# Optimization experiments

Hardware: AMD Instinct MI355X
Metric: run time of the kernel (lower is better)

## Reference

```python
import jax, jax.numpy as jnp
import numpy as np

NUM_ANGLES = 360
IMAGE_SIZE = 256
BATCH = 8


def _radon_forward(x, num_angles=NUM_ANGLES):
    # x: [B, 1, D, D]; replicates torch affine_grid + grid_sample(bilinear,
    # padding_mode='zeros', align_corners=False) followed by mean over rows.
    B = x.shape[0]
    D = x.shape[-1]
    img = x[:, 0]  # [B, D, D]
    angles = jnp.linspace(0.0, 180.0, num_angles + 1, dtype=x.dtype)[:-1]
    t = jnp.deg2rad(angles)
    c, s = jnp.cos(t), jnp.sin(t)
    # align_corners=False normalized pixel-center coords in [-1, 1]
    coords = (2.0 * jnp.arange(D, dtype=x.dtype) + 1.0) / D - 1.0
    xw = coords[None, None, :]   # output x (width)
    yh = coords[None, :, None]   # output y (height)
    cN = c[:, None, None]
    sN = s[:, None, None]
    # theta = [[c, -s, 0], [s, c, 0]] applied to (x_out, y_out, 1)
    gx = cN * xw - sN * yh       # [A, D, D]
    gy = sN * xw + cN * yh
    # unnormalize (align_corners=False)
    ix = ((gx + 1.0) * D - 1.0) * 0.5
    iy = ((gy + 1.0) * D - 1.0) * 0.5
    x0 = jnp.floor(ix)
    y0 = jnp.floor(iy)
    x1 = x0 + 1.0
    y1 = y0 + 1.0
    wx1 = ix - x0
    wx0 = 1.0 - wx1
    wy1 = iy - y0
    wy0 = 1.0 - wy1
    img_flat = img.reshape(B, D * D)

    def corner(xc, yc, w):
        valid = (xc >= 0) & (xc <= D - 1) & (yc >= 0) & (yc <= D - 1)
        xi = jnp.clip(xc, 0, D - 1).astype(jnp.int32)
        yi = jnp.clip(yc, 0, D - 1).astype(jnp.int32)
        lin = yi * D + xi                      # [A, D, D]
        vals = img_flat[:, lin]                # [B, A, D, D]
        return vals * (w * valid.astype(x.dtype))[None]

    rotated = (corner(x0, y0, wx0 * wy0) + corner(x1, y0, wx1 * wy0)
               + corner(x0, y1, wx0 * wy1) + corner(x1, y1, wx1 * wy1))
    proj = rotated.mean(axis=2)                # mean over rows (H) -> [B, A, D]
    return proj[:, None]                       # [B, 1, A, D]


def setup_inputs() -> dict:
    key = jax.random.key(0)
    x = jax.random.normal(key, (BATCH, 1, IMAGE_SIZE, IMAGE_SIZE), dtype=jnp.float32)
    return {"x": x}


def reference(x) -> jnp.ndarray:
    return _radon_forward(x)
```

## Files before the change

### kernel.cpp

```cpp
#include <hip/hip_runtime.h>

#define DD 256
#define BB 8
#define NA 360
#define CH 8
#define HC (DD / CH)
#define TS 32

__device__ __forceinline__ unsigned bf16_rne(float f) {
    unsigned u = __float_as_uint(f);
    return (u + 0x7fffu + ((u >> 16) & 1u)) >> 16;
}
__device__ __forceinline__ unsigned pack2(float a, float b) {
    return bf16_rne(a) | (bf16_rne(b) << 16);
}
__device__ __forceinline__ void ufma(uint4 q, float wgt, float* acc) {
    acc[0] = fmaf(__uint_as_float(q.x << 16),          wgt, acc[0]);
    acc[1] = fmaf(__uint_as_float(q.x & 0xffff0000u),  wgt, acc[1]);
    acc[2] = fmaf(__uint_as_float(q.y << 16),          wgt, acc[2]);
    acc[3] = fmaf(__uint_as_float(q.y & 0xffff0000u),  wgt, acc[3]);
    acc[4] = fmaf(__uint_as_float(q.z << 16),          wgt, acc[4]);
    acc[5] = fmaf(__uint_as_float(q.z & 0xffff0000u),  wgt, acc[5]);
    acc[6] = fmaf(__uint_as_float(q.w << 16),          wgt, acc[6]);
    acc[7] = fmaf(__uint_as_float(q.w & 0xffff0000u),  wgt, acc[7]);
}

__global__ __launch_bounds__(256) void pack_bf16(const float* __restrict__ x,
                                                 uint4* __restrict__ pN,
                                                 uint4* __restrict__ pT) {
    __shared__ uint4 t[TS][TS + 1];
    const int tx = threadIdx.x & 31;
    const int ty = threadIdx.x >> 5;
    const int x0 = (blockIdx.x & 7) * TS;
    const int y0 = (blockIdx.x >> 3) * TS;

#pragma unroll
    for (int r = ty; r < TS; r += 8) {
        const int pix = (y0 + r) * DD + x0 + tx;
        uint4 v;
        v.x = pack2(x[0 * DD * DD + pix], x[1 * DD * DD + pix]);
        v.y = pack2(x[2 * DD * DD + pix], x[3 * DD * DD + pix]);
        v.z = pack2(x[4 * DD * DD + pix], x[5 * DD * DD + pix]);
        v.w = pack2(x[6 * DD * DD + pix], x[7 * DD * DD + pix]);
        pN[pix] = v;
        t[r][tx] = v;
    }
    __syncthreads();
#pragma unroll
    for (int r = ty; r < TS; r += 8)
        pT[(x0 + r) * DD + y0 + tx] = t[tx][r];
}

__global__ __launch_bounds__(256) void radon_bf16(const uint4* __restrict__ pN,
                                                  const uint4* __restrict__ pT,
                                                  float* __restrict__ out) {
    const int a  = blockIdx.x;
    const int hc = blockIdx.y;
    const int w  = threadIdx.x;

    const float ang = (float)a * 0.5f;
    const float t = ang * 0.017453292519943295f;
    const float s = sinf(t);
    const float c = cosf(t);

    const float uw  = (float)w - 127.5f;
    const float axN = fmaf(c, uw, 127.5f);
    const float ayN = fmaf(s, uw, 127.5f);

    const uint4* __restrict__ P;
    float ax, dx, ay, dy;
    if (fabsf(s) <= fabsf(c)) { P = pN; ax = axN; dx = -s; ay = ayN; dy = c;  }
    else                      { P = pT; ax = ayN; dx = c;  ay = axN; dy = -s; }

    float acc[BB];
#pragma unroll
    for (int b = 0; b < BB; ++b) acc[b] = 0.f;

    const int h0 = hc * HC;
#pragma unroll 2
    for (int i = 0; i < HC; ++i) {
        const float uh = (float)(h0 + i) - 127.5f;
        const float ix = fmaf(dx, uh, ax);
        const float iy = fmaf(dy, uh, ay);
        const float x0f = floorf(ix), y0f = floorf(iy);
        const float wx1 = ix - x0f, wy1 = iy - y0f;
        const float wx0 = 1.f - wx1, wy0 = 1.f - wy1;
        const int x0 = (int)x0f, y0 = (int)y0f;
        const float vx0 = ((unsigned)x0 < 256u) ? wx0 : 0.f;
        const float vx1 = ((unsigned)(x0 + 1) < 256u) ? wx1 : 0.f;
        const float vy0 = ((unsigned)y0 < 256u) ? wy0 : 0.f;
        const float vy1 = ((unsigned)(y0 + 1) < 256u) ? wy1 : 0.f;
        const int x0c = min(max(x0, 0), 255);
        const int x1c = min(max(x0 + 1, 0), 255);
        const int y0c = min(max(y0, 0), 255);
        const int y1c = min(max(y0 + 1, 0), 255);
        const float w00 = vx0 * vy0, w10 = vx1 * vy0;
        const float w01 = vx0 * vy1, w11 = vx1 * vy1;

        const uint4 q00 = P[y0c * DD + x0c];
        const uint4 q10 = P[y0c * DD + x1c];
        const uint4 q01 = P[y1c * DD + x0c];
        const uint4 q11 = P[y1c * DD + x1c];

        ufma(q00, w00, acc);
        ufma(q10, w10, acc);
        ufma(q01, w01, acc);
        ufma(q11, w11, acc);
    }

    const float sc = 1.0f / 256.0f;
#pragma unroll
    for (int b = 0; b < BB; ++b)
        atomicAdd(out + (size_t)b * NA * DD + (size_t)a * DD + w, acc[b] * sc);
}

__global__ __launch_bounds__(256) void radon_direct(const float* __restrict__ x,
                                                    float* __restrict__ out) {
    const int a  = blockIdx.x;
    const int hc = blockIdx.y;
    const int w  = threadIdx.x;
    const float ang = (float)a * 0.5f;
    const float t = ang * 0.017453292519943295f;
    const float s = sinf(t);
    const float c = cosf(t);
    const float uw = (float)w - 127.5f;
    const float ax = fmaf(c, uw, 127.5f);
    const float ay = fmaf(s, uw, 127.5f);

    float acc[BB];
#pragma unroll
    for (int b = 0; b < BB; ++b) acc[b] = 0.f;

    const int h0 = hc * HC;
    for (int i = 0; i < HC; ++i) {
        const float uh = (float)(h0 + i) - 127.5f;
        const float ix = fmaf(-s, uh, ax);
        const float iy = fmaf(c, uh, ay);
        const float x0f = floorf(ix), y0f = floorf(iy);
        const float wx1 = ix - x0f, wy1 = iy - y0f;
        const float wx0 = 1.f - wx1, wy0 = 1.f - wy1;
        const int x0 = (int)x0f, y0 = (int)y0f;
        const float vx0 = ((unsigned)x0 < 256u) ? wx0 : 0.f;
        const float vx1 = ((unsigned)(x0 + 1) < 256u) ? wx1 : 0.f;
        const float vy0 = ((unsigned)y0 < 256u) ? wy0 : 0.f;
        const float vy1 = ((unsigned)(y0 + 1) < 256u) ? wy1 : 0.f;
        const int x0c = min(max(x0, 0), 255);
        const int x1c = min(max(x0 + 1, 0), 255);
        const int y0c = min(max(y0, 0), 255);
        const int y1c = min(max(y0 + 1, 0), 255);
        const float w00 = vx0 * vy0, w10 = vx1 * vy0;
        const float w01 = vx0 * vy1, w11 = vx1 * vy1;
        const int l00 = y0c * DD + x0c, l10 = y0c * DD + x1c;
        const int l01 = y1c * DD + x0c, l11 = y1c * DD + x1c;
#pragma unroll
        for (int b = 0; b < BB; ++b) {
            const float* ib = x + (size_t)b * DD * DD;
            acc[b] = fmaf(ib[l00], w00, acc[b]);
            acc[b] = fmaf(ib[l10], w10, acc[b]);
            acc[b] = fmaf(ib[l01], w01, acc[b]);
            acc[b] = fmaf(ib[l11], w11, acc[b]);
        }
    }

    const float sc = 1.0f / 256.0f;
    float* o = out + (size_t)a * DD + w;
#pragma unroll
    for (int b = 0; b < BB; ++b)
        atomicAdd(o + (size_t)b * NA * DD, acc[b] * sc);
}

extern "C" void kernel_launch(void* const* d_in, const int* in_sizes, int n_in,
                              void* d_out, int out_size, void* d_ws, size_t ws_size,
                              hipStream_t stream) {
    const float* x = (const float*)d_in[0];
    float* out = (float*)d_out;

    hipMemsetAsync(d_out, 0, (size_t)out_size * sizeof(float), stream);

    const size_t need = 2ull * DD * DD * sizeof(uint4);
    if (ws_size >= need) {
        uint4* pN = (uint4*)d_ws;
        uint4* pT = pN + (size_t)DD * DD;
        pack_bf16<<<64, 256, 0, stream>>>(x, pN, pT);
        radon_bf16<<<dim3(NA, CH), 256, 0, stream>>>(pN, pT, out);
    } else {
        radon_direct<<<dim3(NA, CH), 256, 0, stream>>>(x, out);
    }
}
```

Measured before the change: 145.4 us.

## Pack image as fp16 x-pairs and use fdot2 for bilinear gathers

Replaces the bf16 per-pixel packing with an fp16 layout that stores each pixel together with its right neighbour for all 8 batches. A second layout offset by one pixel is built by a new derive kernel. The radon kernel then issues two 32-byte row loads instead of four 16-byte corner loads and folds the x-interpolation into packed fdot2 instructions, halving the FMA count. The cost is an extra kernel launch, twice the workspace, and reduced precision: fp16 has a narrower range than bf16 and the packed weights use round-toward-zero conversion.

```diff
diff --git a/kernel.cpp b/kernel.cpp
--- a/kernel.cpp
+++ b/kernel.cpp
@@ -5,55 +5,83 @@
 #define NA 360
 #define CH 8
 #define HC (DD / CH)
-#define TS 32
-
-__device__ __forceinline__ unsigned bf16_rne(float f) {
-    unsigned u = __float_as_uint(f);
-    return (u + 0x7fffu + ((u >> 16) & 1u)) >> 16;
-}
-__device__ __forceinline__ unsigned pack2(float a, float b) {
-    return bf16_rne(a) | (bf16_rne(b) << 16);
-}
-__device__ __forceinline__ void ufma(uint4 q, float wgt, float* acc) {
-    acc[0] = fmaf(__uint_as_float(q.x << 16),          wgt, acc[0]);
-    acc[1] = fmaf(__uint_as_float(q.x & 0xffff0000u),  wgt, acc[1]);
-    acc[2] = fmaf(__uint_as_float(q.y << 16),          wgt, acc[2]);
-    acc[3] = fmaf(__uint_as_float(q.y & 0xffff0000u),  wgt, acc[3]);
-    acc[4] = fmaf(__uint_as_float(q.z << 16),          wgt, acc[4]);
-    acc[5] = fmaf(__uint_as_float(q.z & 0xffff0000u),  wgt, acc[5]);
-    acc[6] = fmaf(__uint_as_float(q.w << 16),          wgt, acc[6]);
-    acc[7] = fmaf(__uint_as_float(q.w & 0xffff0000u),  wgt, acc[7]);
-}
-
-__global__ __launch_bounds__(256) void pack_bf16(const float* __restrict__ x,
-                                                 uint4* __restrict__ pN,
-                                                 uint4* __restrict__ pT) {
-    __shared__ uint4 t[TS][TS + 1];
-    const int tx = threadIdx.x & 31;
-    const int ty = threadIdx.x >> 5;
-    const int x0 = (blockIdx.x & 7) * TS;
-    const int y0 = (blockIdx.x >> 3) * TS;
-
-#pragma unroll
-    for (int r = ty; r < TS; r += 8) {
-        const int pix = (y0 + r) * DD + x0 + tx;
-        uint4 v;
-        v.x = pack2(x[0 * DD * DD + pix], x[1 * DD * DD + pix]);
-        v.y = pack2(x[2 * DD * DD + pix], x[3 * DD * DD + pix]);
-        v.z = pack2(x[4 * DD * DD + pix], x[5 * DD * DD + pix]);
-        v.w = pack2(x[6 * DD * DD + pix], x[7 * DD * DD + pix]);
-        pN[pix] = v;
-        t[r][tx] = v;
-    }
+
+typedef _Float16 half2_t __attribute__((ext_vector_type(2)));
+
+#if defined(__has_builtin)
+#if __has_builtin(__builtin_amdgcn_fdot2)
+#define HAVE_FDOT2 1
+#endif
+#endif
+
+__device__ __forceinline__ float fdot2(unsigned p, half2_t wp, float acc) {
+#ifdef HAVE_FDOT2
+    return __builtin_amdgcn_fdot2(__builtin_bit_cast(half2_t, p), wp, acc, false);
+#else
+    half2_t hp = __builtin_bit_cast(half2_t, p);
+    return acc + (float)hp.x * (float)wp.x + (float)hp.y * (float)wp.y;
+#endif
+}
+
+__device__ __forceinline__ half2_t pkrtz(float a, float b) {
+    return __builtin_bit_cast(half2_t, __builtin_amdgcn_cvt_pkrtz(a, b));
+}
+
+__device__ __forceinline__ unsigned pk_rne(float a, float b) {
+    unsigned short ua = __builtin_bit_cast(unsigned short, (_Float16)a);
+    unsigned short ub = __builtin_bit_cast(unsigned short, (_Float16)b);
+    return (unsigned)ua | ((unsigned)ub << 16);
+}
+
+
+__global__ __launch_bounds__(256) void pack_f16(const float* __restrict__ x,
+                                                char* __restrict__ ws) {
+    __shared__ float t[BB][16][17];
+    const int bx = blockIdx.x & 15, by = blockIdx.x >> 4;
+    const int x0 = bx * 16, y0 = by * 16;
+    const int r0 = threadIdx.x >> 4, c0 = threadIdx.x & 15;
+#pragma unroll
+    for (int b = 0; b < BB; ++b)
+        t[b][r0][c0] = x[b * DD * DD + (y0 + r0) * DD + x0 + c0];
     __syncthreads();
-#pragma unroll
-    for (int r = ty; r < TS; r += 8)
-        pT[(x0 + r) * DD + y0 + tx] = t[tx][r];
-}
-
-__global__ __launch_bounds__(256) void radon_bf16(const uint4* __restrict__ pN,
-                                                  const uint4* __restrict__ pT,
-                                                  float* __restrict__ out) {
+
+    const int r  = threadIdx.x >> 4;
+    const int jj = (threadIdx.x >> 1) & 7;
+    const int h  = threadIdx.x & 1;
+    uint4 vN, vT;
+    unsigned* dN = (unsigned*)&vN;
+    unsigned* dT = (unsigned*)&vT;
+#pragma unroll
+    for (int i = 0; i < 4; ++i) {
+        const int b = 4 * h + i;
+        dN[i] = pk_rne(t[b][r][2 * jj],     t[b][r][2 * jj + 1]);
+        dT[i] = pk_rne(t[b][2 * jj][r],     t[b][2 * jj + 1][r]);
+    }
+    char* pNA = ws;
+    char* pTA = ws + (2u << 20);
+    *(uint4*)(pNA + ((y0 + r) << 12) + ((x0 / 2 + jj) << 5) + h * 16) = vN;
+    *(uint4*)(pTA + ((x0 + r) << 12) + ((y0 / 2 + jj) << 5) + h * 16) = vT;
+}
+
+__global__ __launch_bounds__(256) void derive_B(char* __restrict__ ws) {
+    char* baseA = ws + (size_t)blockIdx.y * (2u << 20);
+    char* baseB = baseA + (1u << 20);
+    const int y = blockIdx.x;
+    const int j = threadIdx.x >> 1;
+    const int h = threadIdx.x & 1;
+    const size_t off = ((size_t)y << 12) + ((size_t)j << 5) + h * 16;
+    uint4 a0 = *(const uint4*)(baseA + off);
+    uint4 a1 = (j < 127) ? *(const uint4*)(baseA + off + 32) : make_uint4(0, 0, 0, 0);
+    uint4 b;
+    b.x = (a0.x >> 16) | (a1.x << 16);
+    b.y = (a0.y >> 16) | (a1.y << 16);
+    b.z = (a0.z >> 16) | (a1.z << 16);
+    b.w = (a0.w >> 16) | (a1.w << 16);
+    *(uint4*)(baseB + off) = b;
+}
+
+__global__ __launch_bounds__(256) void radon_f16(const char* __restrict__ ws,
+                                                 float* __restrict__ out) {
     const int a  = blockIdx.x;
     const int hc = blockIdx.y;
     const int w  = threadIdx.x;
@@ -67,10 +95,10 @@
     const float axN = fmaf(c, uw, 127.5f);
     const float ayN = fmaf(s, uw, 127.5f);
 
-    const uint4* __restrict__ P;
+    const char* __restrict__ P;
     float ax, dx, ay, dy;
-    if (fabsf(s) <= fabsf(c)) { P = pN; ax = axN; dx = -s; ay = ayN; dy = c;  }
-    else                      { P = pT; ax = ayN; dx = c;  ay = axN; dy = -s; }
+    if (fabsf(s) <= fabsf(c)) { P = ws;              ax = axN; dx = -s; ay = ayN; dy = c;  }
+    else                      { P = ws + (2u << 20); ax = ayN; dx = c;  ay = axN; dy = -s; }
 
     float acc[BB];
 #pragma unroll
@@ -86,26 +114,49 @@
         const float wx1 = ix - x0f, wy1 = iy - y0f;
         const float wx0 = 1.f - wx1, wy0 = 1.f - wy1;
         const int x0 = (int)x0f, y0 = (int)y0f;
+
         const float vx0 = ((unsigned)x0 < 256u) ? wx0 : 0.f;
         const float vx1 = ((unsigned)(x0 + 1) < 256u) ? wx1 : 0.f;
+        const bool sx = x0 < 0;
+        const float wAx = sx ? vx1 : vx0;
+        const float wBx = sx ? 0.f : vx1;
+        const int cls = sx ? 0 : (x0 & 1);
+        int j = sx ? 0 : (x0 >> 1);
+        j = min(j, 127);
+
         const float vy0 = ((unsigned)y0 < 256u) ? wy0 : 0.f;
         const float vy1 = ((unsigned)(y0 + 1) < 256u) ? wy1 : 0.f;
-        const int x0c = min(max(x0, 0), 255);
-        const int x1c = min(max(x0 + 1, 0), 255);
-        const int y0c = min(max(y0, 0), 255);
-        const int y1c = min(max(y0 + 1, 0), 255);
-        const float w00 = vx0 * vy0, w10 = vx1 * vy0;
-        const float w01 = vx0 * vy1, w11 = vx1 * vy1;
-
-        const uint4 q00 = P[y0c * DD + x0c];
-        const uint4 q10 = P[y0c * DD + x1c];
-        const uint4 q01 = P[y1c * DD + x0c];
-        const uint4 q11 = P[y1c * DD + x1c];
-
-        ufma(q00, w00, acc);
-        ufma(q10, w10, acc);
-        ufma(q01, w01, acc);
-        ufma(q11, w11, acc);
+        const bool sy = y0 < 0;
+        const float wr0 = sy ? vy1 : vy0;
+        const float wr1 = sy ? 0.f : vy1;
+        const int R0 = min(max(y0, 0), 255);
+        const int R1 = min(max(y0 + 1, 0), 255);
+
+        const half2_t wp0 = pkrtz(wr0 * wAx, wr0 * wBx);
+        const half2_t wp1 = pkrtz(wr1 * wAx, wr1 * wBx);
+
+        const unsigned offx = ((unsigned)cls << 20) | ((unsigned)j << 5);
+        const uint4* e0 = (const uint4*)(P + (offx | ((unsigned)R0 << 12)));
+        const uint4* e1 = (const uint4*)(P + (offx | ((unsigned)R1 << 12)));
+        const uint4 qa0 = e0[0], qb0 = e0[1];
+        const uint4 qa1 = e1[0], qb1 = e1[1];
+
+        acc[0] = fdot2(qa0.x, wp0, acc[0]);
+        acc[1] = fdot2(qa0.y, wp0, acc[1]);
+        acc[2] = fdot2(qa0.z, wp0, acc[2]);
+        acc[3] = fdot2(qa0.w, wp0, acc[3]);
+        acc[4] = fdot2(qb0.x, wp0, acc[4]);
+        acc[5] = fdot2(qb0.y, wp0, acc[5]);
+        acc[6] = fdot2(qb0.z, wp0, acc[6]);
+        acc[7] = fdot2(qb0.w, wp0, acc[7]);
+        acc[0] = fdot2(qa1.x, wp1, acc[0]);
+        acc[1] = fdot2(qa1.y, wp1, acc[1]);
+        acc[2] = fdot2(qa1.z, wp1, acc[2]);
+        acc[3] = fdot2(qa1.w, wp1, acc[3]);
+        acc[4] = fdot2(qb1.x, wp1, acc[4]);
+        acc[5] = fdot2(qb1.y, wp1, acc[5]);
+        acc[6] = fdot2(qb1.z, wp1, acc[6]);
+        acc[7] = fdot2(qb1.w, wp1, acc[7]);
     }
 
     const float sc = 1.0f / 256.0f;
@@ -175,14 +226,14 @@
     const float* x = (const float*)d_in[0];
     float* out = (float*)d_out;
 
-    hipMemsetAsync(d_out, 0, (size_t)out_size * sizeof(float), stream);
-
-    const size_t need = 2ull * DD * DD * sizeof(uint4);
+    (void)hipMemsetAsync(d_out, 0, (size_t)out_size * sizeof(float), stream);
+
+    const size_t need = 4ull << 20;
     if (ws_size >= need) {
-        uint4* pN = (uint4*)d_ws;
-        uint4* pT = pN + (size_t)DD * DD;
-        pack_bf16<<<64, 256, 0, stream>>>(x, pN, pT);
-        radon_bf16<<<dim3(NA, CH), 256, 0, stream>>>(pN, pT, out);
+        char* ws = (char*)d_ws;
+        pack_f16<<<256, 256, 0, stream>>>(x, ws);
+        derive_B<<<dim3(256, 2), 256, 0, stream>>>(ws);
+        radon_f16<<<dim3(NA, CH), 256, 0, stream>>>(ws, out);
     } else {
         radon_direct<<<dim3(NA, CH), 256, 0, stream>>>(x, out);
     }
```

Result: slower. 172.2 us (+18.4%).

## Reduce rows in-block via shared memory, drop memset and atomics, switch to fp16 packing

Applied to the files above, without the earlier changes.

The radon kernel now gives each block a 64-column segment, with four waves each covering an interleaved quarter of the rows. Partial sums are combined in shared memory and written with plain stores, which removes the output memset and the global atomics. Packed storage changes from bf16 to fp16, which keeps more mantissa bits but risks overflow or precision loss for large input values. The new block split also changes the column and row access pattern and the overall grid size.

```diff
diff --git a/kernel.cpp b/kernel.cpp
--- a/kernel.cpp
+++ b/kernel.cpp
@@ -3,60 +3,61 @@
 #define DD 256
 #define BB 8
 #define NA 360
-#define CH 8
-#define HC (DD / CH)
-#define TS 32
 
-__device__ __forceinline__ unsigned bf16_rne(float f) {
-    unsigned u = __float_as_uint(f);
-    return (u + 0x7fffu + ((u >> 16) & 1u)) >> 16;
-}
-__device__ __forceinline__ unsigned pack2(float a, float b) {
-    return bf16_rne(a) | (bf16_rne(b) << 16);
-}
-__device__ __forceinline__ void ufma(uint4 q, float wgt, float* acc) {
-    acc[0] = fmaf(__uint_as_float(q.x << 16),          wgt, acc[0]);
-    acc[1] = fmaf(__uint_as_float(q.x & 0xffff0000u),  wgt, acc[1]);
-    acc[2] = fmaf(__uint_as_float(q.y << 16),          wgt, acc[2]);
-    acc[3] = fmaf(__uint_as_float(q.y & 0xffff0000u),  wgt, acc[3]);
-    acc[4] = fmaf(__uint_as_float(q.z << 16),          wgt, acc[4]);
-    acc[5] = fmaf(__uint_as_float(q.z & 0xffff0000u),  wgt, acc[5]);
-    acc[6] = fmaf(__uint_as_float(q.w << 16),          wgt, acc[6]);
-    acc[7] = fmaf(__uint_as_float(q.w & 0xffff0000u),  wgt, acc[7]);
+typedef _Float16 half2_t __attribute__((ext_vector_type(2)));
+
+__device__ __forceinline__ unsigned pk_f16(float a, float b) {
+    unsigned short ua = __builtin_bit_cast(unsigned short, (_Float16)a);
+    unsigned short ub = __builtin_bit_cast(unsigned short, (_Float16)b);
+    return (unsigned)ua | ((unsigned)ub << 16);
 }
 
-__global__ __launch_bounds__(256) void pack_bf16(const float* __restrict__ x,
-                                                 uint4* __restrict__ pN,
-                                                 uint4* __restrict__ pT) {
-    __shared__ uint4 t[TS][TS + 1];
+__device__ __forceinline__ void mix8(uint4 q, float wgt, float* acc) {
+    half2_t h;
+    h = __builtin_bit_cast(half2_t, q.x);
+    acc[0] = fmaf((float)h.x, wgt, acc[0]); acc[1] = fmaf((float)h.y, wgt, acc[1]);
+    h = __builtin_bit_cast(half2_t, q.y);
+    acc[2] = fmaf((float)h.x, wgt, acc[2]); acc[3] = fmaf((float)h.y, wgt, acc[3]);
+    h = __builtin_bit_cast(half2_t, q.z);
+    acc[4] = fmaf((float)h.x, wgt, acc[4]); acc[5] = fmaf((float)h.y, wgt, acc[5]);
+    h = __builtin_bit_cast(half2_t, q.w);
+    acc[6] = fmaf((float)h.x, wgt, acc[6]); acc[7] = fmaf((float)h.y, wgt, acc[7]);
+}
+
+__global__ __launch_bounds__(256) void pack_f16(const float* __restrict__ x,
+                                                uint4* __restrict__ pN,
+                                                uint4* __restrict__ pT) {
+    __shared__ uint4 t[32][33];
     const int tx = threadIdx.x & 31;
     const int ty = threadIdx.x >> 5;
-    const int x0 = (blockIdx.x & 7) * TS;
-    const int y0 = (blockIdx.x >> 3) * TS;
+    const int x0 = (blockIdx.x & 7) * 32;
+    const int y0 = (blockIdx.x >> 3) * 32;
 
 #pragma unroll
-    for (int r = ty; r < TS; r += 8) {
+    for (int r = ty; r < 32; r += 8) {
         const int pix = (y0 + r) * DD + x0 + tx;
         uint4 v;
-        v.x = pack2(x[0 * DD * DD + pix], x[1 * DD * DD + pix]);
-        v.y = pack2(x[2 * DD * DD + pix], x[3 * DD * DD + pix]);
-        v.z = pack2(x[4 * DD * DD + pix], x[5 * DD * DD + pix]);
-        v.w = pack2(x[6 * DD * DD + pix], x[7 * DD * DD + pix]);
+        v.x = pk_f16(x[0 * DD * DD + pix], x[1 * DD * DD + pix]);
+        v.y = pk_f16(x[2 * DD * DD + pix], x[3 * DD * DD + pix]);
+        v.z = pk_f16(x[4 * DD * DD + pix], x[5 * DD * DD + pix]);
+        v.w = pk_f16(x[6 * DD * DD + pix], x[7 * DD * DD + pix]);
         pN[pix] = v;
         t[r][tx] = v;
     }
     __syncthreads();
 #pragma unroll
-    for (int r = ty; r < TS; r += 8)
+    for (int r = ty; r < 32; r += 8)
         pT[(x0 + r) * DD + y0 + tx] = t[tx][r];
 }
 
-__global__ __launch_bounds__(256) void radon_bf16(const uint4* __restrict__ pN,
-                                                  const uint4* __restrict__ pT,
-                                                  float* __restrict__ out) {
-    const int a  = blockIdx.x;
-    const int hc = blockIdx.y;
-    const int w  = threadIdx.x;
+__global__ __launch_bounds__(256) void radon_mix(const uint4* __restrict__ pN,
+                                                 const uint4* __restrict__ pT,
+                                                 float* __restrict__ out) {
+    const int a    = blockIdx.x;
+    const int wseg = blockIdx.y;
+    const int g    = threadIdx.x >> 6;
+    const int lane = threadIdx.x & 63;
+    const int w    = wseg * 64 + lane;
 
     const float ang = (float)a * 0.5f;
     const float t = ang * 0.017453292519943295f;
@@ -76,10 +77,9 @@
 #pragma unroll
     for (int b = 0; b < BB; ++b) acc[b] = 0.f;
 
-    const int h0 = hc * HC;
 #pragma unroll 2
-    for (int i = 0; i < HC; ++i) {
-        const float uh = (float)(h0 + i) - 127.5f;
+    for (int i = 0; i < 64; ++i) {
+        const float uh = (float)(g + 4 * i) - 127.5f;
         const float ix = fmaf(dx, uh, ax);
         const float iy = fmaf(dy, uh, ay);
         const float x0f = floorf(ix), y0f = floorf(iy);
@@ -102,16 +102,27 @@
         const uint4 q01 = P[y1c * DD + x0c];
         const uint4 q11 = P[y1c * DD + x1c];
 
-        ufma(q00, w00, acc);
-        ufma(q10, w10, acc);
-        ufma(q01, w01, acc);
-        ufma(q11, w11, acc);
+        mix8(q00, w00, acc);
+        mix8(q10, w10, acc);
+        mix8(q01, w01, acc);
+        mix8(q11, w11, acc);
     }
+
+    __shared__ float part[4][64][BB];
+#pragma unroll
+    for (int b = 0; b < BB; b += 4)
+        *(float4*)&part[g][lane][b] = make_float4(acc[b], acc[b + 1], acc[b + 2], acc[b + 3]);
+    __syncthreads();
 
     const float sc = 1.0f / 256.0f;
 #pragma unroll
-    for (int b = 0; b < BB; ++b)
-        atomicAdd(out + (size_t)b * NA * DD + (size_t)a * DD + w, acc[b] * sc);
+    for (int k = 0; k < 2; ++k) {
+        const int id = threadIdx.x + k * 256;
+        const int b  = id >> 6;
+        const int wl = id & 63;
+        const float v = part[0][wl][b] + part[1][wl][b] + part[2][wl][b] + part[3][wl][b];
+        out[(size_t)b * NA * DD + (size_t)a * DD + wseg * 64 + wl] = v * sc;
+    }
 }
 
 __global__ __launch_bounds__(256) void radon_direct(const float* __restrict__ x,
@@ -131,8 +142,8 @@
 #pragma unroll
     for (int b = 0; b < BB; ++b) acc[b] = 0.f;
 
-    const int h0 = hc * HC;
-    for (int i = 0; i < HC; ++i) {
+    const int h0 = hc * 32;
+    for (int i = 0; i < 32; ++i) {
         const float uh = (float)(h0 + i) - 127.5f;
         const float ix = fmaf(-s, uh, ax);
         const float iy = fmaf(c, uh, ay);
@@ -175,15 +186,14 @@
     const float* x = (const float*)d_in[0];
     float* out = (float*)d_out;
 
-    hipMemsetAsync(d_out, 0, (size_t)out_size * sizeof(float), stream);
-
     const size_t need = 2ull * DD * DD * sizeof(uint4);
     if (ws_size >= need) {
         uint4* pN = (uint4*)d_ws;
         uint4* pT = pN + (size_t)DD * DD;
-        pack_bf16<<<64, 256, 0, stream>>>(x, pN, pT);
-        radon_bf16<<<dim3(NA, CH), 256, 0, stream>>>(pN, pT, out);
+        pack_f16<<<64, 256, 0, stream>>>(x, pN, pT);
+        radon_mix<<<dim3(NA, 4), 256, 0, stream>>>(pN, pT, out);
     } else {
-        radon_direct<<<dim3(NA, CH), 256, 0, stream>>>(x, out);
+        (void)hipMemsetAsync(d_out, 0, (size_t)out_size * sizeof(float), stream);
+        radon_direct<<<dim3(NA, 8), 256, 0, stream>>>(x, out);
     }
 }
```

Result: faster. 130.4 us (-10.3%).
